# Optimization experiments

Measured on AMD Instinct MI355X. Metric: run time of the kernel, lower is better.

Reference implementation:

```python
import jax, jax.numpy as jnp
import numpy as np
import math

EMBED_DIM = 1024
NUM_HEADS = 16
HEAD_DIM = EMBED_DIM // NUM_HEADS
ACT_BITS = 8
WGT_BITS = 8


def fake_quant(x, n_bits):
    # Per-tensor symmetric fake quantization with straight-through estimator.
    qmax = 2.0 ** (n_bits - 1) - 1.0  # 127 for 8 bits
    scale = jnp.maximum(jnp.max(jnp.abs(x)) / qmax, 1e-8)
    q = jnp.clip(jnp.round(x / scale), -qmax - 1.0, qmax) * scale
    return x + jax.lax.stop_gradient(q - x)


def setup_inputs() -> dict:
    key = jax.random.key(0)
    ks = jax.random.split(key, 7)
    S, B, D = 2048, 2, EMBED_DIM
    return {
        "query": jax.random.normal(ks[0], (S, B, D), dtype=jnp.float32),
        "key": jax.random.normal(ks[1], (S, B, D), dtype=jnp.float32),
        "value": jax.random.normal(ks[2], (S, B, D), dtype=jnp.float32),
        "Wi": jax.random.normal(ks[3], (3 * D, D), dtype=jnp.float32) * (1.0 / math.sqrt(D)),
        "bi": jax.random.normal(ks[4], (3 * D,), dtype=jnp.float32) * 0.01,
        "Wo": jax.random.normal(ks[5], (D, D), dtype=jnp.float32) * (1.0 / math.sqrt(D)),
        "bo": jax.random.normal(ks[6], (D,), dtype=jnp.float32) * 0.01,
    }


def reference(query, key, value, Wi, bi, Wo, bo):
    D, H, hd = EMBED_DIM, NUM_HEADS, HEAD_DIM
    len_q, batch, _ = query.shape
    len_k = key.shape[0]

    Wi_q = fake_quant(Wi, WGT_BITS)
    Wo_q = fake_quant(Wo, WGT_BITS)

    # in-projections (full 3D projection per input, then chunk, as in source)
    Xq = fake_quant(query @ Wi_q.T + bi, ACT_BITS)
    Xk = fake_quant(key @ Wi_q.T + bi, ACT_BITS)
    Xv = fake_quant(value @ Wi_q.T + bi, ACT_BITS)
    Q = Xq[..., :D]
    K = Xk[..., D:2 * D]
    V = Xv[..., 2 * D:]

    # [len, B, D] -> [B*H, len, hd]
    q = Q.reshape(len_q, batch * H, hd).transpose(1, 0, 2)
    k = K.reshape(len_k, batch * H, hd).transpose(1, 0, 2)
    v = V.reshape(len_k, batch * H, hd).transpose(1, 0, 2)

    q = fake_quant(q / math.sqrt(hd), ACT_BITS)
    attn = jnp.einsum('bqd,bkd->bqk', q, k)  # note: attn/softmax fake-quants in source are no-ops (result discarded)
    attn = jax.nn.softmax(attn, axis=-1)
    heads = fake_quant(jnp.einsum('bqk,bkd->bqd', attn, v), ACT_BITS)

    # [B*H, len_q, hd] -> [len_q*B, D]
    heads_reshape = heads.transpose(1, 0, 2).reshape(len_q * batch, D)
    y = (heads_reshape @ Wo_q.T + bo).reshape(len_q, batch, D)
    return fake_quant(y, ACT_BITS)
```

## Files before the change

### kernel.cpp

```cpp
#include <hip/hip_runtime.h>
#include <math.h>


typedef _Float16 f16;
typedef _Float16 half8 __attribute__((ext_vector_type(8)));
typedef _Float16 half4 __attribute__((ext_vector_type(4)));
typedef _Float16 half2v __attribute__((ext_vector_type(2)));
typedef __fp16 fp16x2 __attribute__((ext_vector_type(2)));
typedef float floatx4 __attribute__((ext_vector_type(4)));
typedef int int4v __attribute__((ext_vector_type(4)));

#define QMAX 127.0f

#define SLOT_WI 0
#define SLOT_WO 1
#define SLOT_XQ 2
#define SLOT_XK 3
#define SLOT_XV 4
#define SLOT_HD 5
#define SLOT_Y  6
#define SLOT_Q  7
#define SLOT_A  8

__device__ __forceinline__ float slot_scale(const unsigned* slots, int slot, float premul) {
  if (slot < 0) return 1.0f;
  return fmaxf(__uint_as_float(slots[slot]) * premul / QMAX, 1e-8f);
}

__device__ __forceinline__ float slot_scaleA(const unsigned* slots) {
  return fmaxf(__uint_as_float(slots[SLOT_A]) / 16256.0f, 1e-8f);
}

__device__ __forceinline__ void gl2lds16(const void* gsrc, void* ldst) {
  __builtin_amdgcn_global_load_lds((__attribute__((address_space(1))) void*)gsrc,
                                   (__attribute__((address_space(3))) void*)ldst, 16, 0, 0);
}

__device__ __forceinline__ half2v pack2(float a, float b) {
  fp16x2 r = __builtin_amdgcn_cvt_pkrtz(a, b);
  return __builtin_bit_cast(half2v, r);
}


__global__ __launch_bounds__(256) void absmax3_k(const float* __restrict__ Wi,
                                                 const float* __restrict__ Wo,
                                                 const float* __restrict__ q,
                                                 const float* __restrict__ k,
                                                 const float* __restrict__ v,
                                                 unsigned* __restrict__ slots) {
  __shared__ float red[256];
  int tid = threadIdx.x;
  int bid = blockIdx.x;
  const float4* x4;
  int n4, i0, stride, slot;
  if (bid < 768) {
    x4 = (const float4*)Wi; n4 = 786432; i0 = bid * 256 + tid;
    stride = 768 * 256; slot = SLOT_WI;
  } else if (bid < 1024) {
    x4 = (const float4*)Wo; n4 = 262144; i0 = (bid - 768) * 256 + tid;
    stride = 256 * 256; slot = SLOT_WO;
  } else {
    int r = bid - 1024;
    int t = r >> 9;
    x4 = (const float4*)(t == 0 ? q : (t == 1 ? k : v));
    n4 = 1048576; i0 = (r & 511) * 256 + tid;
    stride = 512 * 256; slot = SLOT_A;
  }
  float lmax = 0.f;
  for (int i = i0; i < n4; i += stride) {
    float4 vv = x4[i];
    lmax = fmaxf(lmax, fmaxf(fmaxf(fabsf(vv.x), fabsf(vv.y)), fmaxf(fabsf(vv.z), fabsf(vv.w))));
  }
  red[tid] = lmax; __syncthreads();
  for (int sh = 128; sh > 0; sh >>= 1) {
    if (tid < sh) red[tid] = fmaxf(red[tid], red[tid + sh]);
    __syncthreads();
  }
  if (tid == 0) atomicMax(&slots[slot], __float_as_uint(red[0]));
}

__global__ __launch_bounds__(256) void quantw_k(const float* __restrict__ Wi,
                                                const float* __restrict__ Wo,
                                                char* __restrict__ Wi8,
                                                char* __restrict__ Wo8,
                                                const unsigned* __restrict__ slots) {
  int j = blockIdx.x * 256 + threadIdx.x;
  const float* src; char* dst; float s; int a;
  if (j < 196608) {
    s = slot_scale(slots, SLOT_WI, 1.0f); src = Wi; dst = Wi8; a = j;
  } else {
    s = slot_scale(slots, SLOT_WO, 1.0f); src = Wo; dst = Wo8; a = j - 196608;
  }
  int m = ((a >> 10) << 4) | (a & 15);
  int k0 = ((((a >> 6) & 15) << 2) | ((a >> 4) & 3)) << 4;
  const float4* row = (const float4*)(src + (size_t)m * 1024 + k0);
  char ob[16] __attribute__((aligned(16)));
#pragma unroll
  for (int c = 0; c < 4; ++c) {
    float4 x = row[c];
    float xs[4] = {x.x, x.y, x.z, x.w};
#pragma unroll
    for (int u = 0; u < 4; ++u)
      ob[c * 4 + u] = (signed char)(int)fminf(fmaxf(rintf(xs[u] / s), -128.0f), 127.0f);
  }
  *(int4*)(dst + (size_t)a * 16) = *(const int4*)ob;
}

__global__ __launch_bounds__(256) void digitize_k(const float* __restrict__ q,
                                                  const float* __restrict__ k,
                                                  const float* __restrict__ v,
                                                  char* __restrict__ A1,
                                                  char* __restrict__ A2,
                                                  const unsigned* __restrict__ slots) {
  float inv = 1.0f / slot_scaleA(slots);
  int j = blockIdx.x * 256 + threadIdx.x;
  int t = j >> 18;
  int a = j & 262143;
  const float* src = (t == 0 ? q : (t == 1 ? k : v));
  int m = ((a >> 10) << 4) | (a & 15);
  int k0 = ((((a >> 6) & 15) << 2) | ((a >> 4) & 3)) << 4;
  const float4* row = (const float4*)(src + (size_t)m * 1024 + k0);
  char o1[16] __attribute__((aligned(16)));
  char o2[16] __attribute__((aligned(16)));
#pragma unroll
  for (int c = 0; c < 4; ++c) {
    float4 x = row[c];
    float xs[4] = {x.x, x.y, x.z, x.w};
#pragma unroll
    for (int u = 0; u < 4; ++u) {
      float qv = fminf(fmaxf(rintf(xs[u] * inv), -16256.0f), 16256.0f);
      float c1 = rintf(qv * 0.0078125f);
      o1[c * 4 + u] = (signed char)(int)c1;
      o2[c * 4 + u] = (signed char)(int)(qv - 128.0f * c1);
    }
  }
  size_t off = (size_t)t * 4194304 + (size_t)a * 16;
  *(int4*)(A1 + off) = *(const int4*)o1;
  *(int4*)(A2 + off) = *(const int4*)o2;
}

__global__ __launch_bounds__(256) void quantf_k(const float* __restrict__ in, float* __restrict__ out,
                                                int n4, unsigned* __restrict__ slots,
                                                int sSlot, float premul) {
  float s = slot_scale(slots, sSlot, premul);
  const float4* in4 = (const float4*)in;
  float4* out4 = (float4*)out;
  for (int i = blockIdx.x * 256 + threadIdx.x; i < n4; i += gridDim.x * 256) {
    float4 v = in4[i];
    float xs[4] = {v.x, v.y, v.z, v.w};
#pragma unroll
    for (int u = 0; u < 4; ++u) {
      float r = rintf((xs[u] * premul) / s);
      r = fminf(fmaxf(r, -128.0f), 127.0f);
      xs[u] = r * s;
    }
    out4[i] = make_float4(xs[0], xs[1], xs[2], xs[3]);
  }
}

__global__ __launch_bounds__(256) void quanti2_k(const float* __restrict__ Xk,
                                                 f16* __restrict__ Kint,
                                                 const float* __restrict__ Xq,
                                                 f16* __restrict__ Qc,
                                                 unsigned* __restrict__ slots) {
  __shared__ float red[256];
  bool isQ = blockIdx.x >= 1024;
  const float* in = isQ ? Xq : Xk;
  f16* out = isQ ? Qc : Kint;
  float s = slot_scale(slots, isQ ? SLOT_XQ : SLOT_XK, 1.0f);
  int b = isQ ? blockIdx.x - 1024 : blockIdx.x;
  float lmax = 0.f;
  const float4* in4 = (const float4*)in;
  for (int i = b * 256 + threadIdx.x; i < 1048576; i += 1024 * 256) {
    float4 v = in4[i];
    float xs[4] = {v.x, v.y, v.z, v.w};
    half4 o;
#pragma unroll
    for (int u = 0; u < 4; ++u) {
      float r = rintf(xs[u] / s);
      r = fminf(fmaxf(r, -128.0f), 127.0f);
      o[u] = (f16)r;
      lmax = fmaxf(lmax, fabsf(r));
    }
    *(half4*)(out + (size_t)i * 4) = o;
  }
  if (isQ) {
    int tid = threadIdx.x;
    red[tid] = lmax; __syncthreads();
    for (int sh = 128; sh > 0; sh >>= 1) {
      if (tid < sh) red[tid] = fmaxf(red[tid], red[tid + sh]);
      __syncthreads();
    }
    if (tid == 0) atomicMax(&slots[SLOT_Q], __float_as_uint(red[0] * s));
  }
}

__global__ __launch_bounds__(256) void quant8_k(const float* __restrict__ in, char* __restrict__ out,
                                                const unsigned* __restrict__ slots,
                                                int sSlot) {
  float s = slot_scale(slots, sSlot, 1.0f);
  int a = blockIdx.x * 256 + threadIdx.x;
  int m = ((a >> 10) << 4) | (a & 15);
  int k0 = ((((a >> 6) & 15) << 2) | ((a >> 4) & 3)) << 4;
  const float4* row = (const float4*)(in + (size_t)m * 1024 + k0);
  char ob[16] __attribute__((aligned(16)));
#pragma unroll
  for (int c = 0; c < 4; ++c) {
    float4 x = row[c];
    float xs[4] = {x.x, x.y, x.z, x.w};
#pragma unroll
    for (int u = 0; u < 4; ++u)
      ob[c * 4 + u] = (signed char)(int)fminf(fmaxf(rintf(xs[u] / s), -128.0f), 127.0f);
  }
  *(int4*)(out + (size_t)a * 16) = *(const int4*)ob;
}

__global__ __launch_bounds__(256) void quantv_t_k(const float* __restrict__ Xv,
                                                  f16* __restrict__ Vt,
                                                  const unsigned* __restrict__ slots) {
  __shared__ f16 T[64][68];
  int tid = threadIdx.x;
  int bh = blockIdx.y, b = bh >> 4, h = bh & 15;
  int k0 = blockIdx.x * 64;
  float s = slot_scale(slots, SLOT_XV, 1.0f);
#pragma unroll
  for (int it = 0; it < 4; ++it) {
    int idx = tid + it * 256;
    int row = idx >> 4, dseg = idx & 15;
    float4 v = *(const float4*)(Xv + ((size_t)(k0 + row) * 2 + b) * 1024 + h * 64 + dseg * 4);
    float xs[4] = {v.x, v.y, v.z, v.w};
    half4 o;
#pragma unroll
    for (int u = 0; u < 4; ++u) {
      float r = rintf(xs[u] / s);
      o[u] = (f16)fminf(fmaxf(r, -128.0f), 127.0f);
    }
    *(half4*)&T[row][dseg * 4] = o;
  }
  __syncthreads();
#pragma unroll
  for (int it = 0; it < 2; ++it) {
    int sdx = tid + it * 256;
    int d = sdx >> 3, j8 = sdx & 7;
    half8 o;
#pragma unroll
    for (int l = 0; l < 8; ++l) {
      int pos = j8 * 8 + l;
      int tp = pos >> 5, pq = (pos & 31) >> 3, jj = pos & 7;
      int k = tp * 32 + pq * 4 + ((jj < 4) ? jj : jj + 12);
      o[l] = T[k][d];
    }
    *(half8*)(Vt + ((size_t)bh * 64 + d) * 2048 + k0 + j8 * 8) = o;
  }
}

__global__ __launch_bounds__(512) void gemm_qkv_i8_k(const char* __restrict__ A1,
                                                     const char* __restrict__ A2,
                                                     const char* __restrict__ B8,
                                                     const float* __restrict__ bias,
                                                     float* __restrict__ Xout,
                                                     unsigned* __restrict__ slots) {
  __shared__ char As1[2][8192];
  __shared__ char As2[2][8192];
  __shared__ char Bs8[2][8192];
  float* red = (float*)&As1[0][0];

  int tid = threadIdx.x;
  int lane = tid & 63, w = tid >> 6;
  int wm = w >> 1, wn = w & 1;
  int quad = lane >> 4, l15 = lane & 15;
  int t = blockIdx.y >> 5;
  int m0 = (blockIdx.y & 31) * 128;
  int n0 = blockIdx.x * 128;
  size_t aoff = (size_t)t * 4194304;

  const char* a1p = A1 + aoff;
  const char* a2p = A2 + aoff;

  int4v acc1[2][4], acc2[2][4];
#pragma unroll
  for (int i = 0; i < 2; ++i)
#pragma unroll
    for (int j = 0; j < 4; ++j) {
      acc1[i][j] = (int4v){0, 0, 0, 0};
      acc2[i][j] = (int4v){0, 0, 0, 0};
    }

  auto stage = [&](int buf, int kk) __attribute__((always_inline)) {
    size_t ac = ((size_t)((m0 >> 4) + w) << 14) + ((kk >> 6) << 10) + lane * 16;
    size_t bc = ((size_t)((n0 >> 4) + w) << 14) + ((kk >> 6) << 10) + lane * 16;
    gl2lds16(a1p + ac, &As1[buf][w * 1024]);
    gl2lds16(a2p + ac, &As2[buf][w * 1024]);
    gl2lds16(B8 + bc, &Bs8[buf][w * 1024]);
  };

  auto compute = [&](int buf) __attribute__((always_inline)) {
    int4v bf[4];
#pragma unroll
    for (int j = 0; j < 4; ++j)
      bf[j] = *(const int4v*)&Bs8[buf][(wn * 4 + j) * 1024 + lane * 16];
    int4v a1f[2];
#pragma unroll
    for (int i = 0; i < 2; ++i)
      a1f[i] = *(const int4v*)&As1[buf][(wm * 2 + i) * 1024 + lane * 16];
#pragma unroll
    for (int i = 0; i < 2; ++i)
#pragma unroll
      for (int j = 0; j < 4; ++j)
        acc1[i][j] = __builtin_amdgcn_mfma_i32_16x16x64_i8(a1f[i], bf[j], acc1[i][j], 0, 0, 0);
    int4v a2f[2];
#pragma unroll
    for (int i = 0; i < 2; ++i)
      a2f[i] = *(const int4v*)&As2[buf][(wm * 2 + i) * 1024 + lane * 16];
#pragma unroll
    for (int i = 0; i < 2; ++i)
#pragma unroll
      for (int j = 0; j < 4; ++j)
        acc2[i][j] = __builtin_amdgcn_mfma_i32_16x16x64_i8(a2f[i], bf[j], acc2[i][j], 0, 0, 0);
  };

  stage(0, 0);
  __syncthreads();
  for (int kt = 0; kt < 7; ++kt) {
    stage(1, (2 * kt + 1) * 64);
    compute(0);
    __syncthreads();
    stage(0, (2 * kt + 2) * 64);
    compute(1);
    __syncthreads();
  }
  stage(1, 960);
  compute(0);
  __syncthreads();
  compute(1);

  float sc = slot_scaleA(slots) * slot_scale(slots, SLOT_WI, 1.0f);
  int colLo = t * 1024;
  float* outT = Xout + aoff;
  float lmax = 0.f;
#pragma unroll
  for (int i = 0; i < 2; ++i) {
#pragma unroll
    for (int j = 0; j < 4; ++j) {
      int gn = n0 + wn * 64 + j * 16 + l15;
      float bv = bias[gn];
      bool wr = (gn >= colLo && gn < colLo + 1024);
#pragma unroll
      for (int r = 0; r < 4; ++r) {
        int gm = m0 + wm * 32 + i * 16 + quad * 4 + r;
        float vv = fmaf((float)acc1[i][j][r], 128.0f, (float)acc2[i][j][r]) * sc + bv;
        lmax = fmaxf(lmax, fabsf(vv));
        if (wr) outT[(size_t)gm * 1024 + (gn - colLo)] = vv;
      }
    }
  }
  red[tid] = lmax; __syncthreads();
  for (int sh = 256; sh > 0; sh >>= 1) {
    if (tid < sh) red[tid] = fmaxf(red[tid], red[tid + sh]);
    __syncthreads();
  }
  if (tid == 0) atomicMax(&slots[SLOT_XQ + t], __float_as_uint(red[0]));
}

__global__ __launch_bounds__(512) void gemm_i8out_k(const char* __restrict__ A8,
                                                    const char* __restrict__ B8,
                                                    const float* __restrict__ bias,
                                                    float* __restrict__ out,
                                                    unsigned* __restrict__ slots) {
  __shared__ char As8[2][8192];
  __shared__ char Bs8[2][8192];
  float* red = (float*)&As8[0][0];

  int tid = threadIdx.x;
  int lane = tid & 63, w = tid >> 6;
  int wm = w >> 1, wn = w & 1;
  int quad = lane >> 4, l15 = lane & 15;
  int m0 = blockIdx.y * 128, n0 = blockIdx.x * 128;

  int4v acc[2][4];
#pragma unroll
  for (int i = 0; i < 2; ++i)
#pragma unroll
    for (int j = 0; j < 4; ++j) acc[i][j] = (int4v){0, 0, 0, 0};

  auto stage = [&](int buf, int kk) __attribute__((always_inline)) {
    size_t ac = ((size_t)((m0 >> 4) + w) << 14) + ((kk >> 6) << 10) + lane * 16;
    size_t bc = ((size_t)((n0 >> 4) + w) << 14) + ((kk >> 6) << 10) + lane * 16;
    gl2lds16(A8 + ac, &As8[buf][w * 1024]);
    gl2lds16(B8 + bc, &Bs8[buf][w * 1024]);
  };

  auto compute = [&](int buf) __attribute__((always_inline)) {
    int4v bf[4];
#pragma unroll
    for (int j = 0; j < 4; ++j)
      bf[j] = *(const int4v*)&Bs8[buf][(wn * 4 + j) * 1024 + lane * 16];
    int4v af[2];
#pragma unroll
    for (int i = 0; i < 2; ++i)
      af[i] = *(const int4v*)&As8[buf][(wm * 2 + i) * 1024 + lane * 16];
#pragma unroll
    for (int i = 0; i < 2; ++i)
#pragma unroll
      for (int j = 0; j < 4; ++j)
        acc[i][j] = __builtin_amdgcn_mfma_i32_16x16x64_i8(af[i], bf[j], acc[i][j], 0, 0, 0);
  };

  stage(0, 0);
  __syncthreads();
  for (int kt = 0; kt < 7; ++kt) {
    stage(1, (2 * kt + 1) * 64);
    compute(0);
    __syncthreads();
    stage(0, (2 * kt + 2) * 64);
    compute(1);
    __syncthreads();
  }
  stage(1, 960);
  compute(0);
  __syncthreads();
  compute(1);

  float sc = slot_scale(slots, SLOT_HD, 1.0f) * slot_scale(slots, SLOT_WO, 1.0f);
  float lmax = 0.f;
#pragma unroll
  for (int i = 0; i < 2; ++i) {
#pragma unroll
    for (int j = 0; j < 4; ++j) {
      int gn = n0 + wn * 64 + j * 16 + l15;
      float bv = bias[gn];
#pragma unroll
      for (int r = 0; r < 4; ++r) {
        int gm = m0 + wm * 32 + i * 16 + quad * 4 + r;
        float v = (float)acc[i][j][r] * sc + bv;
        lmax = fmaxf(lmax, fabsf(v));
        out[(size_t)gm * 1024 + gn] = v;
      }
    }
  }
  red[tid] = lmax; __syncthreads();
  for (int sh = 256; sh > 0; sh >>= 1) {
    if (tid < sh) red[tid] = fmaxf(red[tid], red[tid + sh]);
    __syncthreads();
  }
  if (tid == 0) atomicMax(&slots[SLOT_Y], __float_as_uint(red[0]));
}

__global__ __launch_bounds__(256) void attn_k(const f16* __restrict__ Qc,
                                              const f16* __restrict__ Kh,
                                              const f16* __restrict__ Vt,
                                              float* __restrict__ heads,
                                              unsigned* __restrict__ slots) {
  __shared__ f16 Ks[64 * 64];
  __shared__ f16 Vs[64][72];
  __shared__ float lred[4][2][16];
  __shared__ float red[256];

  int tid = threadIdx.x;
  int lane = tid & 63, w = tid >> 6;
  int quad = lane >> 4, l15 = lane & 15;
  int bh = blockIdx.y, b = bh >> 4, h = bh & 15;
  int q0 = blockIdx.x * 128;

  float s1 = slot_scale(slots, SLOT_XQ, 1.0f);
  float sq = slot_scale(slots, SLOT_Q, 0.125f);
  float sk = slot_scale(slots, SLOT_XK, 1.0f);
  float sv = slot_scale(slots, SLOT_XV, 1.0f);
  float cS = sq * sk * 1.44269504088896340736f;
  const float FOFF = 12.0f;

  half8 qf[2][2];
#pragma unroll
  for (int s = 0; s < 2; ++s) {
    const f16* qrow = Qc + ((size_t)(q0 + w * 32 + s * 16 + l15) * 2 + b) * 1024 + h * 64;
    half8 qr0 = *(const half8*)(qrow + quad * 8);
    half8 qr1 = *(const half8*)(qrow + 32 + quad * 8);
#pragma unroll
    for (int u = 0; u < 8; ++u) {
      float x0 = ((float)qr0[u] * s1) * 0.125f;
      float x1 = ((float)qr1[u] * s1) * 0.125f;
      qf[s][0][u] = (f16)fminf(fmaxf(rintf(x0 / sq), -128.0f), 127.0f);
      qf[s][1][u] = (f16)fminf(fmaxf(rintf(x1 / sq), -128.0f), 127.0f);
    }
  }

  int ksrow = lane >> 3;
  int ksp = lane & 7;
  int vr0 = tid >> 3, vs0 = (tid & 7) * 8;

  floatx4 oacc[2][4];
#pragma unroll
  for (int s = 0; s < 2; ++s)
#pragma unroll
    for (int d = 0; d < 4; ++d) oacc[s][d] = (floatx4){0.f, 0.f, 0.f, 0.f};
  float lsum[2] = {0.f, 0.f};

  const f16* vbase = Vt + (size_t)bh * 131072;

  for (int kt = 0; kt < 2048; kt += 64) {
    __syncthreads();
#pragma unroll
    for (int t = 0; t < 2; ++t) {
      int r0 = (w * 2 + t) * 8;
      int row = r0 + ksrow;
      int g = ksp ^ (row & 7);
      gl2lds16(Kh + ((size_t)(kt + row) * 2 + b) * 1024 + h * 64 + g * 8, &Ks[r0 * 64]);
    }
    half8 va = *(const half8*)(vbase + (size_t)vr0 * 2048 + kt + vs0);
    half8 vb = *(const half8*)(vbase + (size_t)(vr0 + 32) * 2048 + kt + vs0);
    *(half8*)&Vs[vr0][vs0] = va;
    *(half8*)&Vs[vr0 + 32][vs0] = vb;
    __syncthreads();

    half8 aph[2][2], apl[2][2];
#pragma unroll
    for (int t = 0; t < 4; ++t) {
      int row = t * 16 + l15;
      int g1 = quad ^ (row & 7);
      half8 kf0 = *(half8*)&Ks[row * 64 + g1 * 8];
      half8 kf1 = *(half8*)&Ks[row * 64 + (g1 ^ 4) * 8];
      int tp = t >> 1, hi = (t & 1) * 4;
#pragma unroll
      for (int s = 0; s < 2; ++s) {
        floatx4 sacc = (floatx4){0.f, 0.f, 0.f, 0.f};
        sacc = __builtin_amdgcn_mfma_f32_16x16x32_f16(kf0, qf[s][0], sacc, 0, 0, 0);
        sacc = __builtin_amdgcn_mfma_f32_16x16x32_f16(kf1, qf[s][1], sacc, 0, 0, 0);
        float p0 = __builtin_amdgcn_exp2f(fmaf(sacc[0], cS, -FOFF));
        float p1 = __builtin_amdgcn_exp2f(fmaf(sacc[1], cS, -FOFF));
        float p2 = __builtin_amdgcn_exp2f(fmaf(sacc[2], cS, -FOFF));
        float p3 = __builtin_amdgcn_exp2f(fmaf(sacc[3], cS, -FOFF));
        lsum[s] += (p0 + p1) + (p2 + p3);
        half2v h01 = pack2(p0, p1);
        half2v h23 = pack2(p2, p3);
        half2v l01 = pack2(p0 - (float)h01[0], p1 - (float)h01[1]);
        half2v l23 = pack2(p2 - (float)h23[0], p3 - (float)h23[1]);
        aph[s][tp][hi + 0] = h01[0]; aph[s][tp][hi + 1] = h01[1];
        aph[s][tp][hi + 2] = h23[0]; aph[s][tp][hi + 3] = h23[1];
        apl[s][tp][hi + 0] = l01[0]; apl[s][tp][hi + 1] = l01[1];
        apl[s][tp][hi + 2] = l23[0]; apl[s][tp][hi + 3] = l23[1];
      }
    }

#pragma unroll
    for (int d = 0; d < 4; ++d) {
      const f16* vsrow = &Vs[d * 16 + l15][0];
      half8 b0 = *(const half8*)(vsrow + quad * 8);
      half8 b1 = *(const half8*)(vsrow + 32 + quad * 8);
#pragma unroll
      for (int s = 0; s < 2; ++s) {
        oacc[s][d] = __builtin_amdgcn_mfma_f32_16x16x32_f16(aph[s][0], b0, oacc[s][d], 0, 0, 0);
        oacc[s][d] = __builtin_amdgcn_mfma_f32_16x16x32_f16(apl[s][0], b0, oacc[s][d], 0, 0, 0);
        oacc[s][d] = __builtin_amdgcn_mfma_f32_16x16x32_f16(aph[s][1], b1, oacc[s][d], 0, 0, 0);
        oacc[s][d] = __builtin_amdgcn_mfma_f32_16x16x32_f16(apl[s][1], b1, oacc[s][d], 0, 0, 0);
      }
    }
  }

#pragma unroll
  for (int s = 0; s < 2; ++s) {
    float l = lsum[s];
    l += __shfl_xor(l, 16);
    l += __shfl_xor(l, 32);
    lred[w][s][l15] = l;
  }
  float linv[2][4];
#pragma unroll
  for (int s = 0; s < 2; ++s)
#pragma unroll
    for (int r = 0; r < 4; ++r) linv[s][r] = sv / lred[w][s][quad * 4 + r];

  float lmax = 0.f;
#pragma unroll
  for (int s = 0; s < 2; ++s)
#pragma unroll
    for (int d = 0; d < 4; ++d)
#pragma unroll
      for (int r = 0; r < 4; ++r) {
        float hv = oacc[s][d][r] * linv[s][r];
        heads[((size_t)(q0 + w * 32 + s * 16 + quad * 4 + r) * 2 + b) * 1024 +
              h * 64 + d * 16 + l15] = hv;
        lmax = fmaxf(lmax, fabsf(hv));
      }
  red[tid] = lmax; __syncthreads();
  for (int sh = 128; sh > 0; sh >>= 1) {
    if (tid < sh) red[tid] = fmaxf(red[tid], red[tid + sh]);
    __syncthreads();
  }
  if (tid == 0) atomicMax(&slots[SLOT_HD], __float_as_uint(red[0]));
}

extern "C" void kernel_launch(void* const* d_in, const int* in_sizes, int n_in,
                              void* d_out, int out_size, void* d_ws, size_t ws_size,
                              hipStream_t stream) {
  (void)in_sizes; (void)n_in; (void)out_size; (void)ws_size;
  const float* query = (const float*)d_in[0];
  const float* key   = (const float*)d_in[1];
  const float* value = (const float*)d_in[2];
  const float* Wi    = (const float*)d_in[3];
  const float* bi    = (const float*)d_in[4];
  const float* Wo    = (const float*)d_in[5];
  const float* bo    = (const float*)d_in[6];
  float* out = (float*)d_out;

  char* p = (char*)d_ws;
  unsigned* slots = (unsigned*)p;            p += 1024;
  char* Wi8 = p;                             p += 3072 * 1024;
  char* Wo8 = p;                             p += 1024 * 1024;
  char* A1  = p;                             p += 12288 * 1024;
  char* A2  = p;                             p += 12288 * 1024;
  float* Hd = (float*)A1;
  f16* Kint = (f16*)(A2 + 4194304);
  float* Xq = (float*)p;                     p += 4096 * 1024 * 4;
  float* Y  = Xq;
  float* Xk = (float*)p;                     p += 4096 * 1024 * 4;
  f16* Qc   = (f16*)Xk;
  float* Xv = (float*)p;                     p += 4096 * 1024 * 4;
  char* Hint8 = (char*)Xv + 4096 * 1024 * 2;
  f16* Vt   = (f16*)p;                       p += 4096 * 1024 * 2;

  hipMemsetAsync(slots, 0, 64, stream);
  absmax3_k<<<2560, 256, 0, stream>>>(Wi, Wo, query, key, value, slots);
  quantw_k<<<1024, 256, 0, stream>>>(Wi, Wo, Wi8, Wo8, slots);
  digitize_k<<<3072, 256, 0, stream>>>(query, key, value, A1, A2, slots);

  dim3 gq(24, 96);
  gemm_qkv_i8_k<<<gq, 512, 0, stream>>>(A1, A2, Wi8, bi, Xq, slots);

  quanti2_k<<<2048, 256, 0, stream>>>(Xk, Kint, Xq, Qc, slots);

  dim3 gvt(32, 32);
  quantv_t_k<<<gvt, 256, 0, stream>>>(Xv, Vt, slots);

  dim3 ga(16, 32);
  attn_k<<<ga, 256, 0, stream>>>(Qc, Kint, Vt, Hd, slots);

  quant8_k<<<1024, 256, 0, stream>>>(Hd, Hint8, slots, SLOT_HD);

  dim3 g2(8, 32);
  gemm_i8out_k<<<g2, 512, 0, stream>>>(Hint8, Wo8, bo, Y, slots);

  quantf_k<<<1024, 256, 0, stream>>>(Y, out, 1048576, slots, SLOT_Y, 1.0f);
}
```

Baseline: 375.9 us.

## Double-buffer K/V tiles in attention kernel to overlap loads with MFMA compute

```diff
diff --git a/kernel.cpp b/kernel.cpp
--- a/kernel.cpp
+++ b/kernel.cpp
@@ -451,8 +451,8 @@
                                               const f16* __restrict__ Vt,
                                               float* __restrict__ heads,
                                               unsigned* __restrict__ slots) {
-  __shared__ f16 Ks[64 * 64];
-  __shared__ f16 Vs[64][72];
+  __shared__ f16 Ks[2][64 * 64];
+  __shared__ f16 Vs[2][64][72];
   __shared__ float lred[4][2][16];
   __shared__ float red[256];
 
@@ -496,29 +496,34 @@
   float lsum[2] = {0.f, 0.f};
 
   const f16* vbase = Vt + (size_t)bh * 131072;
-
-  for (int kt = 0; kt < 2048; kt += 64) {
-    __syncthreads();
+  half8 va, vb;
+
+  auto stageK = [&](int bf, int kt) __attribute__((always_inline)) {
 #pragma unroll
     for (int t = 0; t < 2; ++t) {
       int r0 = (w * 2 + t) * 8;
       int row = r0 + ksrow;
       int g = ksp ^ (row & 7);
-      gl2lds16(Kh + ((size_t)(kt + row) * 2 + b) * 1024 + h * 64 + g * 8, &Ks[r0 * 64]);
-    }
-    half8 va = *(const half8*)(vbase + (size_t)vr0 * 2048 + kt + vs0);
-    half8 vb = *(const half8*)(vbase + (size_t)(vr0 + 32) * 2048 + kt + vs0);
-    *(half8*)&Vs[vr0][vs0] = va;
-    *(half8*)&Vs[vr0 + 32][vs0] = vb;
-    __syncthreads();
-
+      gl2lds16(Kh + ((size_t)(kt + row) * 2 + b) * 1024 + h * 64 + g * 8, &Ks[bf][r0 * 64]);
+    }
+  };
+  auto loadV = [&](int kt) __attribute__((always_inline)) {
+    va = *(const half8*)(vbase + (size_t)vr0 * 2048 + kt + vs0);
+    vb = *(const half8*)(vbase + (size_t)(vr0 + 32) * 2048 + kt + vs0);
+  };
+  auto writeV = [&](int bf) __attribute__((always_inline)) {
+    *(half8*)&Vs[bf][vr0][vs0] = va;
+    *(half8*)&Vs[bf][vr0 + 32][vs0] = vb;
+  };
+
+  auto compute = [&](int bf) __attribute__((always_inline)) {
     half8 aph[2][2], apl[2][2];
 #pragma unroll
     for (int t = 0; t < 4; ++t) {
       int row = t * 16 + l15;
       int g1 = quad ^ (row & 7);
-      half8 kf0 = *(half8*)&Ks[row * 64 + g1 * 8];
-      half8 kf1 = *(half8*)&Ks[row * 64 + (g1 ^ 4) * 8];
+      half8 kf0 = *(half8*)&Ks[bf][row * 64 + g1 * 8];
+      half8 kf1 = *(half8*)&Ks[bf][row * 64 + (g1 ^ 4) * 8];
       int tp = t >> 1, hi = (t & 1) * 4;
 #pragma unroll
       for (int s = 0; s < 2; ++s) {
@@ -543,7 +548,7 @@
 
 #pragma unroll
     for (int d = 0; d < 4; ++d) {
-      const f16* vsrow = &Vs[d * 16 + l15][0];
+      const f16* vsrow = &Vs[bf][d * 16 + l15][0];
       half8 b0 = *(const half8*)(vsrow + quad * 8);
       half8 b1 = *(const half8*)(vsrow + 32 + quad * 8);
 #pragma unroll
@@ -554,7 +559,24 @@
         oacc[s][d] = __builtin_amdgcn_mfma_f32_16x16x32_f16(apl[s][1], b1, oacc[s][d], 0, 0, 0);
       }
     }
-  }
+  };
+
+  stageK(0, 0);
+  loadV(0);
+  writeV(0);
+  loadV(64);
+  __syncthreads();
+
+  int buf = 0;
+  for (int it = 0; it < 31; ++it) {
+    stageK(buf ^ 1, (it + 1) * 64);
+    writeV(buf ^ 1);
+    if (it < 30) loadV((it + 2) * 64);
+    compute(buf);
+    __syncthreads();
+    buf ^= 1;
+  }
+  compute(buf);
 
 #pragma unroll
   for (int s = 0; s < 2; ++s) {
```

Result: faster. 359.1 us, median of 2 (-4.5%).
